# Optimization experiments

Hardware: AMD Instinct MI355X
Metric: run time of the kernel (lower is better)

The kernel has to match this reference:

```python
import jax, jax.numpy as jnp
import numpy as np

S = 64        # state_dim
M = 16        # message_dim
H = 128       # hidden_unit_message_dim
HR = 128      # hidden_unit_readout_dim
NSTEPS = 10
N_NODES = 10000
N_FACTORS = 40000


def setup_inputs() -> dict:
    rng = np.random.default_rng(0)
    n, F = N_NODES, N_FACTORS
    # random undirected factor pairs (u, v) with u < v
    u = rng.integers(0, n - 1, F)
    v = rng.integers(u + 1, n)
    # var->factor directed edges: (u, i) and (v, i) for factor i
    v2f_src = np.stack([u, v], 1).ravel().astype(np.int32)          # [E]
    v2f_dst = np.repeat(np.arange(F), 2).astype(np.int32)           # [E]
    b = rng.normal(size=n).astype(np.float32)
    Juv = rng.normal(size=F).astype(np.float32)
    Jvu = rng.normal(size=F).astype(np.float32)
    feat_u = np.stack([b[u], b[v], Juv, Jvu], 1)
    feat_v = np.stack([b[v], b[u], Juv, Jvu], 1)
    feat = np.stack([feat_u, feat_v], 1).reshape(-1, 4).astype(np.float32)  # [E,4]
    p = lambda *s: (0.1 * rng.normal(size=s)).astype(np.float32)
    z = lambda *s: np.zeros(s, np.float32)
    inp = {
        'v2f_src': jnp.asarray(v2f_src), 'v2f_dst': jnp.asarray(v2f_dst),
        'f2v_src': jnp.asarray(v2f_dst), 'f2v_dst': jnp.asarray(v2f_src),
        'feat_v2f': jnp.asarray(feat), 'feat_f2v': jnp.asarray(feat),
        'n_nodes': n, 'n_factors': F,
        'Qw': jnp.asarray(p(4, M * M)), 'Qb': jnp.asarray(z(M * M)),
        'mp1_w1': jnp.asarray(p(2 * S, H)), 'mp1_b1': jnp.asarray(z(H)),
        'mp1_w2': jnp.asarray(p(H, H)), 'mp1_b2': jnp.asarray(z(H)),
        'mp1_w3': jnp.asarray(p(H, M)), 'mp1_b3': jnp.asarray(z(M)),
        'mp2_w1': jnp.asarray(p(2 * S, H)), 'mp2_b1': jnp.asarray(z(H)),
        'mp2_w2': jnp.asarray(p(H, H)), 'mp2_b2': jnp.asarray(z(H)),
        'mp2_w3': jnp.asarray(p(H, M)), 'mp2_b3': jnp.asarray(z(M)),
        'g1_wih': jnp.asarray(p(M, 3 * S)), 'g1_whh': jnp.asarray(p(S, 3 * S)),
        'g1_bih': jnp.asarray(z(3 * S)), 'g1_bhh': jnp.asarray(z(3 * S)),
        'g2_wih': jnp.asarray(p(M, 3 * S)), 'g2_whh': jnp.asarray(p(S, 3 * S)),
        'g2_bih': jnp.asarray(z(3 * S)), 'g2_bhh': jnp.asarray(z(3 * S)),
        'ro_w1': jnp.asarray(p(S, HR)), 'ro_b1': jnp.asarray(z(HR)),
        'ro_w2': jnp.asarray(p(HR, HR)), 'ro_b2': jnp.asarray(z(HR)),
        'ro_w3': jnp.asarray(p(HR, 2)), 'ro_b3': jnp.asarray(z(2)),
    }
    return inp


def _mlp(x, w1, b1, w2, b2, w3, b3):
    h = jax.nn.relu(x @ w1 + b1)
    h = jax.nn.relu(h @ w2 + b2)
    return h @ w3 + b3


def _gru(x, h, wih, whh, bih, bhh):
    # torch.nn.GRUCell gate order: r, z, n
    gi = x @ wih + bih
    gh = h @ whh + bhh
    ir, iz, inn = jnp.split(gi, 3, axis=-1)
    hr, hz, hn = jnp.split(gh, 3, axis=-1)
    r = jax.nn.sigmoid(ir + hr)
    zg = jax.nn.sigmoid(iz + hz)
    ng = jnp.tanh(inn + r * hn)
    return (1.0 - zg) * ng + zg * h


def reference(v2f_src, v2f_dst, f2v_src, f2v_dst, feat_v2f, feat_f2v,
              n_nodes, n_factors, Qw, Qb,
              mp1_w1, mp1_b1, mp1_w2, mp1_b2, mp1_w3, mp1_b3,
              mp2_w1, mp2_b1, mp2_w2, mp2_b2, mp2_w3, mp2_b3,
              g1_wih, g1_whh, g1_bih, g1_bhh,
              g2_wih, g2_whh, g2_bih, g2_bhh,
              ro_w1, ro_b1, ro_w2, ro_b2, ro_w3, ro_b3):
    var_h = jnp.zeros((n_nodes, S), feat_v2f.dtype)
    fac_h = jnp.zeros((n_factors, S), feat_v2f.dtype)
    # per-edge transform matrices are the same every step; hoist out of the loop
    q1 = (feat_v2f @ Qw + Qb).reshape(-1, M, M)  # [E, M, M]
    q2 = (feat_f2v @ Qw + Qb).reshape(-1, M, M)
    for _ in range(NSTEPS):
        # var -> factor
        x = jnp.concatenate([var_h[v2f_src], fac_h[v2f_dst]], axis=-1)  # [E, 2S]
        m = _mlp(x, mp1_w1, mp1_b1, mp1_w2, mp1_b2, mp1_w3, mp1_b3)    # [E, M]
        m = jnp.einsum('eij,ej->ei', q1, m)
        fac_msg = jax.ops.segment_sum(m, v2f_dst, num_segments=n_factors)
        fac_h = _gru(fac_msg, fac_h, g1_wih, g1_whh, g1_bih, g1_bhh)
        # factor -> var
        x = jnp.concatenate([fac_h[f2v_src], var_h[f2v_dst]], axis=-1)
        m = _mlp(x, mp2_w1, mp2_b1, mp2_w2, mp2_b2, mp2_w3, mp2_b3)
        m = jnp.einsum('eij,ej->ei', q2, m)
        var_msg = jax.ops.segment_sum(m, f2v_dst, num_segments=n_nodes)
        var_h = _gru(var_msg, var_h, g2_wih, g2_whh, g2_bih, g2_bhh)
    out = _mlp(var_h, ro_w1, ro_b1, ro_w2, ro_b2, ro_w3, ro_b3)  # [n_nodes, 2]
    return jax.nn.softmax(out, axis=1)
```

## Files before the change

### kernel.cpp

```cpp
#include <hip/hip_runtime.h>

#define NSTEPS 10

typedef __attribute__((ext_vector_type(8))) short bf16x8;
typedef __attribute__((ext_vector_type(4))) short bf16x4;
typedef __attribute__((ext_vector_type(4))) float f32x4;

__device__ __forceinline__ float sigmoidf_(float x) { return 1.0f / (1.0f + __expf(-x)); }
__device__ __forceinline__ float tanh_fast(float x) {
  const float e = __expf(2.f * x);
  return 1.f - 2.f / (e + 1.f);
}

__device__ __forceinline__ short bf16_(float x) {
  union { float f; unsigned u; } c; c.f = x;
  unsigned r = (c.u + 0x7FFFu + ((c.u >> 16) & 1u)) >> 16;
  return (short)r;
}
__device__ __forceinline__ unsigned pk2_(float a, float b) {
  union { float f; unsigned u; } ca, cb; ca.f = a; cb.f = b;
  return __builtin_amdgcn_perm(cb.u + 0x8000u, ca.u + 0x8000u, 0x07060302u);
}
__device__ __forceinline__ short pk1_(float a) {
  union { float f; unsigned u; } c; c.f = a;
  return (short)((c.u + 0x8000u) >> 16);
}
__device__ __forceinline__ float lo_(unsigned u) { union { unsigned u; float f; } c; c.u = u << 16; return c.f; }
__device__ __forceinline__ float hi_(unsigned u) { union { unsigned u; float f; } c; c.u = u & 0xffff0000u; return c.f; }

__device__ __forceinline__ f32x4 mfma_16x16x32(bf16x8 a, bf16x8 b, f32x4 c) {
  return __builtin_amdgcn_mfma_f32_16x16x32_bf16(a, b, c, 0, 0, 0);
}

struct PackJob { const float* src; int N; int KS; int nchunks; };
struct PackArgs {
  PackJob jb[10];
  const float* Qw; const float* Qb;
  const float* g1wih; const float* g1whh;
  const float* g2wih; const float* g2whh;
};

__global__ __launch_bounds__(256) void k_pack(PackArgs a, short* __restrict__ out, int total) {
  const int g = blockIdx.x * 256 + threadIdx.x;
  if (g >= total) return;
  int c = g >> 9;
  const int r = g & 511;
  const int j = r & 7, n = (r >> 3) & 15, q = (r >> 7) & 3;
  const int kq = q * 8 + j;
  float val = 0.f;
  bool done = false;
  #pragma unroll
  for (int ji = 0; ji < 10; ++ji) {
    if (!done && c < a.jb[ji].nchunks) {
      const int ks = c % a.jb[ji].KS;
      const int nt = c / a.jb[ji].KS;
      const int k = ks * 32 + kq;
      val = a.jb[ji].src[(size_t)k * a.jb[ji].N + nt * 16 + n];
      done = true;
    }
    if (!done) c -= a.jb[ji].nchunks;
  }
  if (!done) {
    if (c < 5) {
      val = 0.f;
      if (kq < 16) val = (c < 4) ? a.Qw[c * 256 + n * 16 + kq] : a.Qb[n * 16 + kq];
    } else {
      c -= 5;
      const float* wih = (c < 48) ? a.g1wih : a.g2wih;
      const float* whh = (c < 48) ? a.g1whh : a.g2whh;
      if (c >= 48) c -= 48;
      const int nt = c / 3, ks = c % 3;
      const int k = ks * 32 + kq;
      const int ng = nt * 16 + n;
      const int gate = ng >> 6, s = ng & 63;
      val = 0.f;
      if (gate == 0) {
        if (k < 16) val = wih[k * 192 + s];
        else if (k < 80) val = whh[(k - 16) * 192 + s];
      } else if (gate == 1) {
        if (k < 16) val = wih[k * 192 + 64 + s];
        else if (k < 80) val = whh[(k - 16) * 192 + 64 + s];
      } else if (gate == 2) {
        if (k < 16) val = wih[k * 192 + 128 + s];
      } else {
        if (k >= 16 && k < 80) val = whh[(k - 16) * 192 + 128 + s];
      }
    }
  }
  out[g] = bf16_(val);
}

__global__ __launch_bounds__(256) void k_dense2(
    const float* __restrict__ X0, const short* __restrict__ W0, short* __restrict__ C0,
    int rows0, int g0,
    const float* __restrict__ X1, const short* __restrict__ W1, short* __restrict__ C1,
    int rows1, float* __restrict__ zeroPtr)
{
  constexpr int KS = 2, K = 64, STR = K + 8;
  __shared__ short Xs[64 * STR];
  const int t = threadIdx.x, lane = t & 63, wave = t >> 6;

  const float* X; const short* Wf; short* C; int rows, rbase;
  if ((int)blockIdx.x < g0) {
    X = X0; Wf = W0; C = C0; rows = rows0; rbase = blockIdx.x * 64;
  } else {
    X = X1; Wf = W1; C = C1; rows = rows1; rbase = ((int)blockIdx.x - g0) * 64;
    if (zeroPtr) {
      const int zr = rbase + (t >> 2);
      if (zr < rows1) {
        f32x4 z = {0.f, 0.f, 0.f, 0.f};
        *(f32x4*)(zeroPtr + (size_t)zr * 16 + (t & 3) * 4) = z;
      }
    }
  }

  bf16x8 b[2][KS];
  #pragma unroll
  for (int nt2 = 0; nt2 < 2; ++nt2)
    #pragma unroll
    for (int ks = 0; ks < KS; ++ks)
      b[nt2][ks] = ((const bf16x8*)Wf)[((wave * 2 + nt2) * KS + ks) * 64 + lane];

  {
    const int r = t >> 2, q4 = t & 3, rg = rbase + r;
    #pragma unroll
    for (int i = 0; i < K / 16; ++i) {
      const int cc = q4 * 4 + i * 16;
      f32x4 v = {0.f, 0.f, 0.f, 0.f};
      if (rg < rows) v = *(const f32x4*)(X + (size_t)rg * K + cc);
      *(unsigned*)&Xs[r * STR + cc]     = pk2_(v.x, v.y);
      *(unsigned*)&Xs[r * STR + cc + 2] = pk2_(v.z, v.w);
    }
  }
  __syncthreads();

  const int m = lane & 15, quad = lane >> 4;
  f32x4 acc[2][4] = {};
  #pragma unroll
  for (int ks = 0; ks < KS; ++ks) {
    bf16x8 afr[4];
    #pragma unroll
    for (int mt = 0; mt < 4; ++mt)
      afr[mt] = *(const bf16x8*)&Xs[(mt * 16 + m) * STR + ks * 32 + quad * 8];
    #pragma unroll
    for (int nt2 = 0; nt2 < 2; ++nt2)
      #pragma unroll
      for (int mt = 0; mt < 4; ++mt)
        acc[nt2][mt] = mfma_16x16x32(afr[mt], b[nt2][ks], acc[nt2][mt]);
  }

  #pragma unroll
  for (int nt2 = 0; nt2 < 2; ++nt2) {
    const int col = (wave * 2 + nt2) * 16 + m;
    #pragma unroll
    for (int mt = 0; mt < 4; ++mt)
      #pragma unroll
      for (int rr = 0; rr < 4; ++rr) {
        const int rg = rbase + mt * 16 + quad * 4 + rr;
        if (rg < rows) C[(size_t)rg * 128 + col] = pk1_(acc[nt2][mt][rr]);
      }
  }
}

template<int KS>
__global__ __launch_bounds__(256) void k_dense(
    const float* __restrict__ X, const short* __restrict__ Wf,
    const float* __restrict__ bias, float* __restrict__ C, int rows)
{
  constexpr int K = KS * 32;
  constexpr int STR = K + 8;
  __shared__ short Xs[64 * STR];
  const int t = threadIdx.x, lane = t & 63, wave = t >> 6;
  const int rbase = blockIdx.x * 64;

  bf16x8 b[2][KS];
  #pragma unroll
  for (int nt2 = 0; nt2 < 2; ++nt2)
    #pragma unroll
    for (int ks = 0; ks < KS; ++ks)
      b[nt2][ks] = ((const bf16x8*)Wf)[((wave * 2 + nt2) * KS + ks) * 64 + lane];

  {
    const int r = t >> 2, q4 = t & 3, rg = rbase + r;
    #pragma unroll
    for (int i = 0; i < K / 16; ++i) {
      const int cc = q4 * 4 + i * 16;
      f32x4 v = {0.f, 0.f, 0.f, 0.f};
      if (rg < rows) v = *(const f32x4*)(X + (size_t)rg * K + cc);
      *(unsigned*)&Xs[r * STR + cc]     = pk2_(v.x, v.y);
      *(unsigned*)&Xs[r * STR + cc + 2] = pk2_(v.z, v.w);
    }
  }
  __syncthreads();

  const int m = lane & 15, quad = lane >> 4;
  f32x4 acc[2][4] = {};
  #pragma unroll
  for (int ks = 0; ks < KS; ++ks) {
    bf16x8 afr[4];
    #pragma unroll
    for (int mt = 0; mt < 4; ++mt)
      afr[mt] = *(const bf16x8*)&Xs[(mt * 16 + m) * STR + ks * 32 + quad * 8];
    #pragma unroll
    for (int nt2 = 0; nt2 < 2; ++nt2)
      #pragma unroll
      for (int mt = 0; mt < 4; ++mt)
        acc[nt2][mt] = mfma_16x16x32(afr[mt], b[nt2][ks], acc[nt2][mt]);
  }

  #pragma unroll
  for (int nt2 = 0; nt2 < 2; ++nt2) {
    const int col = (wave * 2 + nt2) * 16 + m;
    const float bv = bias[col];
    #pragma unroll
    for (int mt = 0; mt < 4; ++mt)
      #pragma unroll
      for (int rr = 0; rr < 4; ++rr) {
        const int rg = rbase + mt * 16 + quad * 4 + rr;
        if (rg < rows) C[(size_t)rg * 128 + col] = fmaxf(acc[nt2][mt][rr] + bv, 0.f);
      }
  }
}

template<bool PAIRED>
__global__ __launch_bounds__(256) void k_edge(
    const short* __restrict__ Pa, const short* __restrict__ Pb,
    const int* __restrict__ src, const int* __restrict__ dst,
    const float* __restrict__ feat,
    const float* __restrict__ b1, const float* __restrict__ b2,
    const float* __restrict__ b3,
    const short* __restrict__ w2f, const short* __restrict__ w3f,
    const short* __restrict__ qf,
    float* __restrict__ outMsg, int E)
{
  __shared__ short h1s[64 * 136];
  __shared__ short ms[64 * 40];
  __shared__ float feats[64 * 4];
  __shared__ int sidx[64], didx[64];

  const int t = threadIdx.x, lane = t & 63, wave = t >> 6;
  const int e0 = blockIdx.x * 64;

  if (t < 64) {
    const int eg = e0 + t;
    sidx[t] = (eg < E) ? src[eg] : 0;
    didx[t] = (eg < E) ? dst[eg] : 0;
  }
  {
    const int e = t >> 2, k = t & 3;
    const int eg = e0 + e;
    feats[e * 4 + k] = (eg < E) ? feat[(size_t)eg * 4 + k] : 0.f;
  }
  bf16x8 bw2[2][4];
  #pragma unroll
  for (int nt2 = 0; nt2 < 2; ++nt2)
    #pragma unroll
    for (int ks = 0; ks < 4; ++ks)
      bw2[nt2][ks] = ((const bf16x8*)w2f)[((wave * 2 + nt2) * 4 + ks) * 64 + lane];
  __syncthreads();

  {
    const int r = t >> 2, q4 = t & 3;
    const bool ok = (e0 + r) < E;
    const short* pa = Pa + (size_t)sidx[r] * 128;
    const short* pb = Pb + (size_t)didx[r] * 128;
    #pragma unroll
    for (int i = 0; i < 4; ++i) {
      const int col = (q4 + i * 4) * 8;
      uint4 o = make_uint4(0u, 0u, 0u, 0u);
      if (ok) {
        const uint4 ua = *(const uint4*)(pa + col);
        const uint4 ub = *(const uint4*)(pb + col);
        const f32x4 ba = *(const f32x4*)(b1 + col);
        const f32x4 bb = *(const f32x4*)(b1 + col + 4);
        o.x = pk2_(fmaxf(lo_(ua.x) + lo_(ub.x) + ba.x, 0.f),
                   fmaxf(hi_(ua.x) + hi_(ub.x) + ba.y, 0.f));
        o.y = pk2_(fmaxf(lo_(ua.y) + lo_(ub.y) + ba.z, 0.f),
                   fmaxf(hi_(ua.y) + hi_(ub.y) + ba.w, 0.f));
        o.z = pk2_(fmaxf(lo_(ua.z) + lo_(ub.z) + bb.x, 0.f),
                   fmaxf(hi_(ua.z) + hi_(ub.z) + bb.y, 0.f));
        o.w = pk2_(fmaxf(lo_(ua.w) + lo_(ub.w) + bb.z, 0.f),
                   fmaxf(hi_(ua.w) + hi_(ub.w) + bb.w, 0.f));
      }
      *(uint4*)&h1s[r * 136 + col] = o;
    }
  }
  __syncthreads();

  const int m = lane & 15, quad = lane >> 4;

  f32x4 acc2[2][4] = {};
  #pragma unroll
  for (int ks = 0; ks < 4; ++ks) {
    bf16x8 afr[4];
    #pragma unroll
    for (int mt = 0; mt < 4; ++mt)
      afr[mt] = *(const bf16x8*)&h1s[(mt * 16 + m) * 136 + ks * 32 + quad * 8];
    #pragma unroll
    for (int nt2 = 0; nt2 < 2; ++nt2)
      #pragma unroll
      for (int mt = 0; mt < 4; ++mt)
        acc2[nt2][mt] = mfma_16x16x32(afr[mt], bw2[nt2][ks], acc2[nt2][mt]);
  }
  __syncthreads();

  #pragma unroll
  for (int nt2 = 0; nt2 < 2; ++nt2) {
    const int col = (wave * 2 + nt2) * 16 + m;
    const float bv = b2[col];
    #pragma unroll
    for (int mt = 0; mt < 4; ++mt)
      #pragma unroll
      for (int rr = 0; rr < 4; ++rr)
        h1s[(mt * 16 + quad * 4 + rr) * 136 + col] =
            pk1_(fmaxf(acc2[nt2][mt][rr] + bv, 0.f));
  }
  bf16x8 bw3[4];
  #pragma unroll
  for (int ks = 0; ks < 4; ++ks) bw3[ks] = ((const bf16x8*)w3f)[ks * 64 + lane];
  bf16x8 bq[5];
  #pragma unroll
  for (int tq = 0; tq < 5; ++tq) bq[tq] = ((const bf16x8*)qf)[tq * 64 + lane];
  __syncthreads();

  f32x4 acc3 = {};
  #pragma unroll
  for (int ks = 0; ks < 4; ++ks) {
    const bf16x8 afr = *(const bf16x8*)&h1s[(wave * 16 + m) * 136 + ks * 32 + quad * 8];
    acc3 = mfma_16x16x32(afr, bw3[ks], acc3);
  }
  const float b3v = b3[m];
  #pragma unroll
  for (int rr = 0; rr < 4; ++rr) {
    const int row = wave * 16 + quad * 4 + rr;
    ms[row * 40 + m] = pk1_(acc3[rr] + b3v);
    ms[row * 40 + 16 + m] = 0;
  }
  __syncthreads();

  f32x4 accY[5] = {};
  {
    const bf16x8 afr = *(const bf16x8*)&ms[(wave * 16 + m) * 40 + quad * 8];
    #pragma unroll
    for (int tq = 0; tq < 5; ++tq) accY[tq] = mfma_16x16x32(afr, bq[tq], accY[tq]);
  }
  float mq[4];
  #pragma unroll
  for (int rr = 0; rr < 4; ++rr) {
    const int row = wave * 16 + quad * 4 + rr;
    const f32x4 f = *(const f32x4*)&feats[row * 4];
    mq[rr] = accY[4][rr] + f.x * accY[0][rr] + f.y * accY[1][rr]
                         + f.z * accY[2][rr] + f.w * accY[3][rr];
  }

  if (PAIRED) {
    const int erow = wave * 16 + quad * 4;
    const int eg = e0 + erow;
    if (eg < E) {
      const int fb = eg >> 1;
      outMsg[(size_t)fb * 16 + m]       = mq[0] + mq[1];
      outMsg[(size_t)(fb + 1) * 16 + m] = mq[2] + mq[3];
    }
  } else {
    #pragma unroll
    for (int rr = 0; rr < 4; ++rr) {
      const int erow = wave * 16 + quad * 4 + rr;
      if (e0 + erow < E)
        atomicAdd(outMsg + (size_t)didx[erow] * 16 + m, mq[rr]);
    }
  }
}

__global__ __launch_bounds__(256) void k_gru(
    const float* __restrict__ msg, float* __restrict__ h,
    const short* __restrict__ Wf,
    const float* __restrict__ bih, const float* __restrict__ bhh, int rows)
{
  __shared__ short As[64 * 104];
  const int t = threadIdx.x, lane = t & 63, wave = t >> 6;
  const int rbase = blockIdx.x * 64;

  {
    const int r = t >> 2, q4 = t & 3, rg = rbase + r;
    #pragma unroll
    for (int i = 0; i < 6; ++i) {
      const int c = (q4 + i * 4) * 4;
      f32x4 v = {0.f, 0.f, 0.f, 0.f};
      if (rg < rows) {
        if (c < 16)      v = *(const f32x4*)(msg + (size_t)rg * 16 + c);
        else if (c < 80) v = *(const f32x4*)(h + (size_t)rg * 64 + (c - 16));
      }
      *(unsigned*)&As[r * 104 + c]     = pk2_(v.x, v.y);
      *(unsigned*)&As[r * 104 + c + 2] = pk2_(v.z, v.w);
    }
  }
  __syncthreads();

  const int m = lane & 15, quad = lane >> 4;
  f32x4 acc[16] = {};
  #pragma unroll
  for (int ks = 0; ks < 3; ++ks) {
    const bf16x8 a = *(const bf16x8*)&As[(wave * 16 + m) * 104 + ks * 32 + quad * 8];
    #pragma unroll
    for (int nt = 0; nt < 16; ++nt) {
      const bf16x8 b = ((const bf16x8*)Wf)[(nt * 3 + ks) * 64 + lane];
      acc[nt] = mfma_16x16x32(a, b, acc[nt]);
    }
  }

  #pragma unroll
  for (int nt = 0; nt < 4; ++nt) {
    const int s = nt * 16 + m;
    const float br  = bih[s] + bhh[s];
    const float bz  = bih[64 + s] + bhh[64 + s];
    const float bin = bih[128 + s];
    const float bhn = bhh[128 + s];
    #pragma unroll
    for (int reg = 0; reg < 4; ++reg) {
      const int rg = rbase + wave * 16 + quad * 4 + reg;
      if (rg < rows) {
        const float ho = h[(size_t)rg * 64 + s];
        const float rr = sigmoidf_(acc[nt][reg] + br);
        const float zz = sigmoidf_(acc[4 + nt][reg] + bz);
        const float nn = tanh_fast(acc[8 + nt][reg] + bin + rr * (acc[12 + nt][reg] + bhn));
        h[(size_t)rg * 64 + s] = (1.f - zz) * nn + zz * ho;
      }
    }
  }
}

__global__ __launch_bounds__(256) void k_readout(
    const float* __restrict__ T2, const float* __restrict__ w3,
    const float* __restrict__ b3, float* __restrict__ out, int rows)
{
  const int n = blockIdx.x * 256 + threadIdx.x;
  if (n >= rows) return;
  float l0 = b3[0], l1 = b3[1];
  #pragma unroll 8
  for (int k = 0; k < 128; k += 4) {
    const float4 x = *(const float4*)(T2 + (size_t)n * 128 + k);
    l0 = fmaf(x.x, w3[(k + 0) * 2 + 0], l0);
    l0 = fmaf(x.y, w3[(k + 1) * 2 + 0], l0);
    l0 = fmaf(x.z, w3[(k + 2) * 2 + 0], l0);
    l0 = fmaf(x.w, w3[(k + 3) * 2 + 0], l0);
    l1 = fmaf(x.x, w3[(k + 0) * 2 + 1], l1);
    l1 = fmaf(x.y, w3[(k + 1) * 2 + 1], l1);
    l1 = fmaf(x.z, w3[(k + 2) * 2 + 1], l1);
    l1 = fmaf(x.w, w3[(k + 3) * 2 + 1], l1);
  }
  const float mx = fmaxf(l0, l1);
  const float e0 = __expf(l0 - mx), e1 = __expf(l1 - mx);
  const float inv = 1.f / (e0 + e1);
  out[(size_t)n * 2 + 0] = e0 * inv;
  out[(size_t)n * 2 + 1] = e1 * inv;
}

extern "C" void kernel_launch(void* const* d_in, const int* in_sizes, int n_in,
                              void* d_out, int out_size, void* d_ws, size_t ws_size,
                              hipStream_t stream)
{
  const int*   v2f_src  = (const int*)d_in[0];
  const int*   v2f_dst  = (const int*)d_in[1];
  const int*   f2v_src  = (const int*)d_in[2];
  const int*   f2v_dst  = (const int*)d_in[3];
  const float* feat_v2f = (const float*)d_in[4];
  const float* feat_f2v = (const float*)d_in[5];
  const float* Qw    = (const float*)d_in[8];
  const float* Qb    = (const float*)d_in[9];
  const float* m1w1  = (const float*)d_in[10];
  const float* m1b1  = (const float*)d_in[11];
  const float* m1w2  = (const float*)d_in[12];
  const float* m1b2  = (const float*)d_in[13];
  const float* m1w3  = (const float*)d_in[14];
  const float* m1b3  = (const float*)d_in[15];
  const float* m2w1  = (const float*)d_in[16];
  const float* m2b1  = (const float*)d_in[17];
  const float* m2w2  = (const float*)d_in[18];
  const float* m2b2  = (const float*)d_in[19];
  const float* m2w3  = (const float*)d_in[20];
  const float* m2b3  = (const float*)d_in[21];
  const float* g1wih = (const float*)d_in[22];
  const float* g1whh = (const float*)d_in[23];
  const float* g1bih = (const float*)d_in[24];
  const float* g1bhh = (const float*)d_in[25];
  const float* g2wih = (const float*)d_in[26];
  const float* g2whh = (const float*)d_in[27];
  const float* g2bih = (const float*)d_in[28];
  const float* g2bhh = (const float*)d_in[29];
  const float* row1  = (const float*)d_in[30];
  const float* rob1  = (const float*)d_in[31];
  const float* row2  = (const float*)d_in[32];
  const float* rob2  = (const float*)d_in[33];
  const float* row3  = (const float*)d_in[34];
  const float* rob3  = (const float*)d_in[35];

  const int E = in_sizes[0];
  const int N = out_size / 2;
  const int F = E / 2;

  float* ws    = (float*)d_ws;
  float* var_h = ws;
  float* fac_h = var_h + (size_t)N * 64;
  float* msgF  = fac_h + (size_t)F * 64;
  float* msgV  = msgF  + (size_t)F * 16;
  float* T1    = msgV  + (size_t)N * 16;
  float* T2    = T1    + (size_t)N * 128;
  short* Abuf  = (short*)(T2 + (size_t)N * 128);
  short* Bbuf  = Abuf + (size_t)F * 128;
  short* wb    = Bbuf + (size_t)F * 128;

  const int C_W2A = 0,  C_W2B = 32, C_W3A = 64, C_W3B = 68;
  const int C_W1AS = 72, C_W1AD = 88, C_W1BS = 104, C_W1BD = 120;
  const int C_RO1 = 136, C_RO2 = 152, C_Q = 184, C_G1 = 189, C_G2 = 237;
  const int TOTAL_CHUNKS = 285;

  short* PB_w2a  = wb + C_W2A  * 512;
  short* PB_w2b  = wb + C_W2B  * 512;
  short* PB_w3a  = wb + C_W3A  * 512;
  short* PB_w3b  = wb + C_W3B  * 512;
  short* PB_w1as = wb + C_W1AS * 512;
  short* PB_w1ad = wb + C_W1AD * 512;
  short* PB_w1bs = wb + C_W1BS * 512;
  short* PB_w1bd = wb + C_W1BD * 512;
  short* PB_ro1  = wb + C_RO1  * 512;
  short* PB_ro2  = wb + C_RO2  * 512;
  short* PB_q    = wb + C_Q    * 512;
  short* PB_g1   = wb + C_G1   * 512;
  short* PB_g2   = wb + C_G2   * 512;

  hipMemsetAsync(var_h, 0, (size_t)N * 64 * sizeof(float), stream);
  hipMemsetAsync(fac_h, 0, (size_t)F * 64 * sizeof(float), stream);

  PackArgs pa;
  pa.jb[0] = {m1w2,            128, 4, 32};
  pa.jb[1] = {m2w2,            128, 4, 32};
  pa.jb[2] = {m1w3,             16, 4,  4};
  pa.jb[3] = {m2w3,             16, 4,  4};
  pa.jb[4] = {m1w1,            128, 2, 16};
  pa.jb[5] = {m1w1 + 64 * 128, 128, 2, 16};
  pa.jb[6] = {m2w1,            128, 2, 16};
  pa.jb[7] = {m2w1 + 64 * 128, 128, 2, 16};
  pa.jb[8] = {row1,            128, 2, 16};
  pa.jb[9] = {row2,            128, 4, 32};
  pa.Qw = Qw; pa.Qb = Qb;
  pa.g1wih = g1wih; pa.g1whh = g1whh;
  pa.g2wih = g2wih; pa.g2whh = g2whh;
  const int packTotal = TOTAL_CHUNKS * 512;
  k_pack<<<(packTotal + 255) / 256, 256, 0, stream>>>(pa, wb, packTotal);

  const int gN = (N + 63) / 64;
  const int gF = (F + 63) / 64;
  const int gE = (E + 63) / 64;

  for (int step = 0; step < NSTEPS; ++step) {
    k_dense2<<<gN + gF, 256, 0, stream>>>(var_h, PB_w1as, Abuf, N, gN,
                                          fac_h, PB_w1ad, Bbuf, F, nullptr);
    k_edge<true><<<gE, 256, 0, stream>>>(Abuf, Bbuf, v2f_src, v2f_dst, feat_v2f,
                                         m1b1, m1b2, m1b3, PB_w2a, PB_w3a, PB_q, msgF, E);
    k_gru<<<gF, 256, 0, stream>>>(msgF, fac_h, PB_g1, g1bih, g1bhh, F);
    k_dense2<<<gF + gN, 256, 0, stream>>>(fac_h, PB_w1bs, Abuf, F, gF,
                                          var_h, PB_w1bd, Bbuf, N, msgV);
    k_edge<false><<<gE, 256, 0, stream>>>(Abuf, Bbuf, f2v_src, f2v_dst, feat_f2v,
                                          m2b1, m2b2, m2b3, PB_w2b, PB_w3b, PB_q, msgV, E);
    k_gru<<<gN, 256, 0, stream>>>(msgV, var_h, PB_g2, g2bih, g2bhh, N);
  }

  k_dense<2><<<gN, 256, 0, stream>>>(var_h, PB_ro1, rob1, T1, N);
  k_dense<4><<<gN, 256, 0, stream>>>(T1,    PB_ro2, rob2, T2, N);
  k_readout<<<(N + 255) / 256, 256, 0, stream>>>(T2, row3, rob3, (float*)d_out, N);
}
```

Before: 825.1 us.

## Fuse GRU updates into edge and dense kernels and fuse readout MLP

The factor GRU now runs at the end of the paired edge kernel. Each block owns 32 consecutive factors, so it can reduce the message pair in LDS and update fac_h directly, with no msgF buffer. The variable GRU is deferred into the job0 blocks of the next step's dense kernel, and the final step's GRU is folded into one readout kernel that also chains the two dense layers and the softmax through LDS. This removes the standalone GRU and readout launches and the global round-trips for msgF, T1 and T2. The cost is more LDS and register pressure per block and extra MFMA work inside the edge kernel.

```diff
diff --git a/kernel.cpp b/kernel.cpp
--- a/kernel.cpp
+++ b/kernel.cpp
@@ -94,14 +94,20 @@
     const float* __restrict__ X0, const short* __restrict__ W0, short* __restrict__ C0,
     int rows0, int g0,
     const float* __restrict__ X1, const short* __restrict__ W1, short* __restrict__ C1,
-    int rows1, float* __restrict__ zeroPtr)
+    int rows1, float* __restrict__ zeroPtr,
+    const float* __restrict__ gruMsg, float* __restrict__ gruH,
+    const short* __restrict__ gruW,
+    const float* __restrict__ gbih, const float* __restrict__ gbhh)
 {
   constexpr int KS = 2, K = 64, STR = K + 8;
   __shared__ short Xs[64 * STR];
+  __shared__ short SA[64 * 104];
   const int t = threadIdx.x, lane = t & 63, wave = t >> 6;
+  const int m = lane & 15, quad = lane >> 4;
 
   const float* X; const short* Wf; short* C; int rows, rbase;
-  if ((int)blockIdx.x < g0) {
+  const bool job0 = (int)blockIdx.x < g0;
+  if (job0) {
     X = X0; Wf = W0; C = C0; rows = rows0; rbase = blockIdx.x * 64;
   } else {
     X = X1; Wf = W1; C = C1; rows = rows1; rbase = ((int)blockIdx.x - g0) * 64;
@@ -121,7 +127,56 @@
     for (int ks = 0; ks < KS; ++ks)
       b[nt2][ks] = ((const bf16x8*)Wf)[((wave * 2 + nt2) * KS + ks) * 64 + lane];
 
-  {
+  if (job0 && gruMsg) {
+    {
+      const int r = t >> 2, q4 = t & 3, rg = rbase + r;
+      #pragma unroll
+      for (int i = 0; i < 6; ++i) {
+        const int c = q4 * 4 + i * 16;
+        f32x4 v = {0.f, 0.f, 0.f, 0.f};
+        if (rg < rows) {
+          if (c < 16)      v = *(const f32x4*)(gruMsg + (size_t)rg * 16 + c);
+          else if (c < 80) v = *(const f32x4*)(gruH + (size_t)rg * 64 + (c - 16));
+        }
+        *(unsigned*)&SA[r * 104 + c]     = pk2_(v.x, v.y);
+        *(unsigned*)&SA[r * 104 + c + 2] = pk2_(v.z, v.w);
+      }
+    }
+    __syncthreads();
+    f32x4 acc[16] = {};
+    #pragma unroll
+    for (int ks = 0; ks < 3; ++ks) {
+      const bf16x8 a = *(const bf16x8*)&SA[(wave * 16 + m) * 104 + ks * 32 + quad * 8];
+      #pragma unroll
+      for (int nt = 0; nt < 16; ++nt)
+        acc[nt] = mfma_16x16x32(a, ((const bf16x8*)gruW)[(nt * 3 + ks) * 64 + lane], acc[nt]);
+    }
+    #pragma unroll
+    for (int nt = 0; nt < 4; ++nt) {
+      const int s = nt * 16 + m;
+      const float br  = gbih[s] + gbhh[s];
+      const float bz  = gbih[64 + s] + gbhh[64 + s];
+      const float bin = gbih[128 + s];
+      const float bhn = gbhh[128 + s];
+      #pragma unroll
+      for (int reg = 0; reg < 4; ++reg) {
+        const int lr = wave * 16 + quad * 4 + reg;
+        const int rg = rbase + lr;
+        short hv = 0;
+        if (rg < rows) {
+          const float ho = gruH[(size_t)rg * 64 + s];
+          const float rr = sigmoidf_(acc[nt][reg] + br);
+          const float zz = sigmoidf_(acc[4 + nt][reg] + bz);
+          const float nn = tanh_fast(acc[8 + nt][reg] + bin + rr * (acc[12 + nt][reg] + bhn));
+          const float hn = (1.f - zz) * nn + zz * ho;
+          gruH[(size_t)rg * 64 + s] = hn;
+          hv = pk1_(hn);
+        }
+        Xs[lr * STR + s] = hv;
+      }
+    }
+    __syncthreads();
+  } else {
     const int r = t >> 2, q4 = t & 3, rg = rbase + r;
     #pragma unroll
     for (int i = 0; i < K / 16; ++i) {
@@ -131,10 +186,9 @@
       *(unsigned*)&Xs[r * STR + cc]     = pk2_(v.x, v.y);
       *(unsigned*)&Xs[r * STR + cc + 2] = pk2_(v.z, v.w);
     }
-  }
-  __syncthreads();
-
-  const int m = lane & 15, quad = lane >> 4;
+    __syncthreads();
+  }
+
   f32x4 acc[2][4] = {};
   #pragma unroll
   for (int ks = 0; ks < KS; ++ks) {
@@ -158,66 +212,6 @@
       for (int rr = 0; rr < 4; ++rr) {
         const int rg = rbase + mt * 16 + quad * 4 + rr;
         if (rg < rows) C[(size_t)rg * 128 + col] = pk1_(acc[nt2][mt][rr]);
-      }
-  }
-}
-
-template<int KS>
-__global__ __launch_bounds__(256) void k_dense(
-    const float* __restrict__ X, const short* __restrict__ Wf,
-    const float* __restrict__ bias, float* __restrict__ C, int rows)
-{
-  constexpr int K = KS * 32;
-  constexpr int STR = K + 8;
-  __shared__ short Xs[64 * STR];
-  const int t = threadIdx.x, lane = t & 63, wave = t >> 6;
-  const int rbase = blockIdx.x * 64;
-
-  bf16x8 b[2][KS];
-  #pragma unroll
-  for (int nt2 = 0; nt2 < 2; ++nt2)
-    #pragma unroll
-    for (int ks = 0; ks < KS; ++ks)
-      b[nt2][ks] = ((const bf16x8*)Wf)[((wave * 2 + nt2) * KS + ks) * 64 + lane];
-
-  {
-    const int r = t >> 2, q4 = t & 3, rg = rbase + r;
-    #pragma unroll
-    for (int i = 0; i < K / 16; ++i) {
-      const int cc = q4 * 4 + i * 16;
-      f32x4 v = {0.f, 0.f, 0.f, 0.f};
-      if (rg < rows) v = *(const f32x4*)(X + (size_t)rg * K + cc);
-      *(unsigned*)&Xs[r * STR + cc]     = pk2_(v.x, v.y);
-      *(unsigned*)&Xs[r * STR + cc + 2] = pk2_(v.z, v.w);
-    }
-  }
-  __syncthreads();
-
-  const int m = lane & 15, quad = lane >> 4;
-  f32x4 acc[2][4] = {};
-  #pragma unroll
-  for (int ks = 0; ks < KS; ++ks) {
-    bf16x8 afr[4];
-    #pragma unroll
-    for (int mt = 0; mt < 4; ++mt)
-      afr[mt] = *(const bf16x8*)&Xs[(mt * 16 + m) * STR + ks * 32 + quad * 8];
-    #pragma unroll
-    for (int nt2 = 0; nt2 < 2; ++nt2)
-      #pragma unroll
-      for (int mt = 0; mt < 4; ++mt)
-        acc[nt2][mt] = mfma_16x16x32(afr[mt], b[nt2][ks], acc[nt2][mt]);
-  }
-
-  #pragma unroll
-  for (int nt2 = 0; nt2 < 2; ++nt2) {
-    const int col = (wave * 2 + nt2) * 16 + m;
-    const float bv = bias[col];
-    #pragma unroll
-    for (int mt = 0; mt < 4; ++mt)
-      #pragma unroll
-      for (int rr = 0; rr < 4; ++rr) {
-        const int rg = rbase + mt * 16 + quad * 4 + rr;
-        if (rg < rows) C[(size_t)rg * 128 + col] = fmaxf(acc[nt2][mt][rr] + bv, 0.f);
       }
   }
 }
@@ -231,15 +225,20 @@
     const float* __restrict__ b3,
     const short* __restrict__ w2f, const short* __restrict__ w3f,
     const short* __restrict__ qf,
-    float* __restrict__ outMsg, int E)
+    float* __restrict__ outMsg,
+    float* __restrict__ facH, const short* __restrict__ gruW,
+    const float* __restrict__ gbih, const float* __restrict__ gbhh,
+    int E, int F)
 {
   __shared__ short h1s[64 * 136];
   __shared__ short ms[64 * 40];
+  __shared__ short AsG[32 * 104];
   __shared__ float feats[64 * 4];
   __shared__ int sidx[64], didx[64];
 
   const int t = threadIdx.x, lane = t & 63, wave = t >> 6;
   const int e0 = blockIdx.x * 64;
+  const int f0 = e0 >> 1;
 
   if (t < 64) {
     const int eg = e0 + t;
@@ -250,6 +249,23 @@
     const int e = t >> 2, k = t & 3;
     const int eg = e0 + e;
     feats[e * 4 + k] = (eg < E) ? feat[(size_t)eg * 4 + k] : 0.f;
+  }
+  if (PAIRED) {
+    const int hr = t >> 3, hc = (t & 7) * 8;
+    const int f = f0 + hr;
+    f32x4 a0 = {0.f,0.f,0.f,0.f}, a1 = {0.f,0.f,0.f,0.f};
+    if (f < F) {
+      a0 = *(const f32x4*)(facH + (size_t)f * 64 + hc);
+      a1 = *(const f32x4*)(facH + (size_t)f * 64 + hc + 4);
+    }
+    uint4 o;
+    o.x = pk2_(a0.x, a0.y); o.y = pk2_(a0.z, a0.w);
+    o.z = pk2_(a1.x, a1.y); o.w = pk2_(a1.z, a1.w);
+    *(uint4*)&AsG[hr * 104 + 16 + hc] = o;
+    if (t < 64) {
+      uint4 z = make_uint4(0u, 0u, 0u, 0u);
+      *(uint4*)&AsG[(t >> 1) * 104 + 80 + (t & 1) * 8] = z;
+    }
   }
   bf16x8 bw2[2][4];
   #pragma unroll
@@ -354,12 +370,46 @@
   }
 
   if (PAIRED) {
-    const int erow = wave * 16 + quad * 4;
-    const int eg = e0 + erow;
-    if (eg < E) {
-      const int fb = eg >> 1;
-      outMsg[(size_t)fb * 16 + m]       = mq[0] + mq[1];
-      outMsg[(size_t)(fb + 1) * 16 + m] = mq[2] + mq[3];
+    {
+      const int fl = wave * 8 + quad * 2;
+      AsG[fl * 104 + m]       = pk1_(mq[0] + mq[1]);
+      AsG[(fl + 1) * 104 + m] = pk1_(mq[2] + mq[3]);
+    }
+    __syncthreads();
+    const int mt = wave >> 1, sh = wave & 1;
+    f32x4 accG[8] = {};
+    #pragma unroll
+    for (int ks = 0; ks < 3; ++ks) {
+      const bf16x8 a = *(const bf16x8*)&AsG[(mt * 16 + m) * 104 + ks * 32 + quad * 8];
+      #pragma unroll
+      for (int g = 0; g < 4; ++g)
+        #pragma unroll
+        for (int nt2 = 0; nt2 < 2; ++nt2) {
+          const int nt = g * 4 + sh * 2 + nt2;
+          accG[g * 2 + nt2] =
+              mfma_16x16x32(a, ((const bf16x8*)gruW)[(nt * 3 + ks) * 64 + lane],
+                            accG[g * 2 + nt2]);
+        }
+    }
+    #pragma unroll
+    for (int nt2 = 0; nt2 < 2; ++nt2) {
+      const int s = sh * 32 + nt2 * 16 + m;
+      const float br  = gbih[s] + gbhh[s];
+      const float bz  = gbih[64 + s] + gbhh[64 + s];
+      const float bin = gbih[128 + s];
+      const float bhn = gbhh[128 + s];
+      #pragma unroll
+      for (int reg = 0; reg < 4; ++reg) {
+        const int f = f0 + mt * 16 + quad * 4 + reg;
+        if (f < F) {
+          const float ho = facH[(size_t)f * 64 + s];
+          const float rr = sigmoidf_(accG[nt2][reg] + br);
+          const float zz = sigmoidf_(accG[2 + nt2][reg] + bz);
+          const float nn = tanh_fast(accG[4 + nt2][reg] + bin +
+                                     rr * (accG[6 + nt2][reg] + bhn));
+          facH[(size_t)f * 64 + s] = (1.f - zz) * nn + zz * ho;
+        }
+      }
     }
   } else {
     #pragma unroll
@@ -371,88 +421,155 @@
   }
 }
 
-__global__ __launch_bounds__(256) void k_gru(
-    const float* __restrict__ msg, float* __restrict__ h,
-    const short* __restrict__ Wf,
-    const float* __restrict__ bih, const float* __restrict__ bhh, int rows)
+__global__ __launch_bounds__(256) void k_readout_f(
+    const float* __restrict__ gruMsg, const float* __restrict__ gruH,
+    const short* __restrict__ gruW,
+    const float* __restrict__ gbih, const float* __restrict__ gbhh,
+    const short* __restrict__ ro1f, const float* __restrict__ rob1,
+    const short* __restrict__ ro2f, const float* __restrict__ rob2,
+    const float* __restrict__ row3, const float* __restrict__ rob3,
+    float* __restrict__ out, int rows)
 {
-  __shared__ short As[64 * 104];
+  __shared__ short SA[64 * 104];
+  __shared__ short SH[64 * 72];
+  __shared__ short S1[64 * 136];
+  __shared__ short S2[64 * 136];
+  __shared__ float w3s[256];
   const int t = threadIdx.x, lane = t & 63, wave = t >> 6;
+  const int m = lane & 15, quad = lane >> 4;
   const int rbase = blockIdx.x * 64;
+
+  w3s[t] = row3[t];
 
   {
     const int r = t >> 2, q4 = t & 3, rg = rbase + r;
     #pragma unroll
     for (int i = 0; i < 6; ++i) {
-      const int c = (q4 + i * 4) * 4;
+      const int c = q4 * 4 + i * 16;
       f32x4 v = {0.f, 0.f, 0.f, 0.f};
       if (rg < rows) {
-        if (c < 16)      v = *(const f32x4*)(msg + (size_t)rg * 16 + c);
-        else if (c < 80) v = *(const f32x4*)(h + (size_t)rg * 64 + (c - 16));
-      }
-      *(unsigned*)&As[r * 104 + c]     = pk2_(v.x, v.y);
-      *(unsigned*)&As[r * 104 + c + 2] = pk2_(v.z, v.w);
-    }
-  }
-  __syncthreads();
-
-  const int m = lane & 15, quad = lane >> 4;
-  f32x4 acc[16] = {};
-  #pragma unroll
-  for (int ks = 0; ks < 3; ++ks) {
-    const bf16x8 a = *(const bf16x8*)&As[(wave * 16 + m) * 104 + ks * 32 + quad * 8];
-    #pragma unroll
-    for (int nt = 0; nt < 16; ++nt) {
-      const bf16x8 b = ((const bf16x8*)Wf)[(nt * 3 + ks) * 64 + lane];
-      acc[nt] = mfma_16x16x32(a, b, acc[nt]);
-    }
-  }
-
-  #pragma unroll
-  for (int nt = 0; nt < 4; ++nt) {
-    const int s = nt * 16 + m;
-    const float br  = bih[s] + bhh[s];
-    const float bz  = bih[64 + s] + bhh[64 + s];
-    const float bin = bih[128 + s];
-    const float bhn = bhh[128 + s];
-    #pragma unroll
-    for (int reg = 0; reg < 4; ++reg) {
-      const int rg = rbase + wave * 16 + quad * 4 + reg;
-      if (rg < rows) {
-        const float ho = h[(size_t)rg * 64 + s];
-        const float rr = sigmoidf_(acc[nt][reg] + br);
-        const float zz = sigmoidf_(acc[4 + nt][reg] + bz);
-        const float nn = tanh_fast(acc[8 + nt][reg] + bin + rr * (acc[12 + nt][reg] + bhn));
-        h[(size_t)rg * 64 + s] = (1.f - zz) * nn + zz * ho;
-      }
-    }
-  }
-}
-
-__global__ __launch_bounds__(256) void k_readout(
-    const float* __restrict__ T2, const float* __restrict__ w3,
-    const float* __restrict__ b3, float* __restrict__ out, int rows)
-{
-  const int n = blockIdx.x * 256 + threadIdx.x;
-  if (n >= rows) return;
-  float l0 = b3[0], l1 = b3[1];
-  #pragma unroll 8
-  for (int k = 0; k < 128; k += 4) {
-    const float4 x = *(const float4*)(T2 + (size_t)n * 128 + k);
-    l0 = fmaf(x.x, w3[(k + 0) * 2 + 0], l0);
-    l0 = fmaf(x.y, w3[(k + 1) * 2 + 0], l0);
-    l0 = fmaf(x.z, w3[(k + 2) * 2 + 0], l0);
-    l0 = fmaf(x.w, w3[(k + 3) * 2 + 0], l0);
-    l1 = fmaf(x.x, w3[(k + 0) * 2 + 1], l1);
-    l1 = fmaf(x.y, w3[(k + 1) * 2 + 1], l1);
-    l1 = fmaf(x.z, w3[(k + 2) * 2 + 1], l1);
-    l1 = fmaf(x.w, w3[(k + 3) * 2 + 1], l1);
-  }
-  const float mx = fmaxf(l0, l1);
-  const float e0 = __expf(l0 - mx), e1 = __expf(l1 - mx);
-  const float inv = 1.f / (e0 + e1);
-  out[(size_t)n * 2 + 0] = e0 * inv;
-  out[(size_t)n * 2 + 1] = e1 * inv;
+        if (c < 16)      v = *(const f32x4*)(gruMsg + (size_t)rg * 16 + c);
+        else if (c < 80) v = *(const f32x4*)(gruH + (size_t)rg * 64 + (c - 16));
+      }
+      *(unsigned*)&SA[r * 104 + c]     = pk2_(v.x, v.y);
+      *(unsigned*)&SA[r * 104 + c + 2] = pk2_(v.z, v.w);
+    }
+  }
+  __syncthreads();
+  {
+    f32x4 acc[16] = {};
+    #pragma unroll
+    for (int ks = 0; ks < 3; ++ks) {
+      const bf16x8 a = *(const bf16x8*)&SA[(wave * 16 + m) * 104 + ks * 32 + quad * 8];
+      #pragma unroll
+      for (int nt = 0; nt < 16; ++nt)
+        acc[nt] = mfma_16x16x32(a, ((const bf16x8*)gruW)[(nt * 3 + ks) * 64 + lane], acc[nt]);
+    }
+    #pragma unroll
+    for (int nt = 0; nt < 4; ++nt) {
+      const int s = nt * 16 + m;
+      const float br  = gbih[s] + gbhh[s];
+      const float bz  = gbih[64 + s] + gbhh[64 + s];
+      const float bin = gbih[128 + s];
+      const float bhn = gbhh[128 + s];
+      #pragma unroll
+      for (int reg = 0; reg < 4; ++reg) {
+        const int lr = wave * 16 + quad * 4 + reg;
+        const int rg = rbase + lr;
+        short hv = 0;
+        if (rg < rows) {
+          const float ho = gruH[(size_t)rg * 64 + s];
+          const float rr = sigmoidf_(acc[nt][reg] + br);
+          const float zz = sigmoidf_(acc[4 + nt][reg] + bz);
+          const float nn = tanh_fast(acc[8 + nt][reg] + bin + rr * (acc[12 + nt][reg] + bhn));
+          hv = pk1_((1.f - zz) * nn + zz * ho);
+        }
+        SH[lr * 72 + s] = hv;
+      }
+    }
+  }
+  __syncthreads();
+
+  {
+    f32x4 acc[2][4] = {};
+    #pragma unroll
+    for (int ks = 0; ks < 2; ++ks) {
+      bf16x8 afr[4];
+      #pragma unroll
+      for (int mt = 0; mt < 4; ++mt)
+        afr[mt] = *(const bf16x8*)&SH[(mt * 16 + m) * 72 + ks * 32 + quad * 8];
+      #pragma unroll
+      for (int nt2 = 0; nt2 < 2; ++nt2) {
+        const bf16x8 bb = ((const bf16x8*)ro1f)[((wave * 2 + nt2) * 2 + ks) * 64 + lane];
+        #pragma unroll
+        for (int mt = 0; mt < 4; ++mt)
+          acc[nt2][mt] = mfma_16x16x32(afr[mt], bb, acc[nt2][mt]);
+      }
+    }
+    #pragma unroll
+    for (int nt2 = 0; nt2 < 2; ++nt2) {
+      const int col = (wave * 2 + nt2) * 16 + m;
+      const float bv = rob1[col];
+      #pragma unroll
+      for (int mt = 0; mt < 4; ++mt)
+        #pragma unroll
+        for (int rr = 0; rr < 4; ++rr)
+          S1[(mt * 16 + quad * 4 + rr) * 136 + col] =
+              pk1_(fmaxf(acc[nt2][mt][rr] + bv, 0.f));
+    }
+  }
+  __syncthreads();
+
+  {
+    f32x4 acc[2][4] = {};
+    #pragma unroll
+    for (int ks = 0; ks < 4; ++ks) {
+      bf16x8 afr[4];
+      #pragma unroll
+      for (int mt = 0; mt < 4; ++mt)
+        afr[mt] = *(const bf16x8*)&S1[(mt * 16 + m) * 136 + ks * 32 + quad * 8];
+      #pragma unroll
+      for (int nt2 = 0; nt2 < 2; ++nt2) {
+        const bf16x8 bb = ((const bf16x8*)ro2f)[((wave * 2 + nt2) * 4 + ks) * 64 + lane];
+        #pragma unroll
+        for (int mt = 0; mt < 4; ++mt)
+          acc[nt2][mt] = mfma_16x16x32(afr[mt], bb, acc[nt2][mt]);
+      }
+    }
+    #pragma unroll
+    for (int nt2 = 0; nt2 < 2; ++nt2) {
+      const int col = (wave * 2 + nt2) * 16 + m;
+      const float bv = rob2[col];
+      #pragma unroll
+      for (int mt = 0; mt < 4; ++mt)
+        #pragma unroll
+        for (int rr = 0; rr < 4; ++rr)
+          S2[(mt * 16 + quad * 4 + rr) * 136 + col] =
+              pk1_(fmaxf(acc[nt2][mt][rr] + bv, 0.f));
+    }
+  }
+  __syncthreads();
+
+  if (t < 64) {
+    const int rg = rbase + t;
+    if (rg < rows) {
+      float l0 = rob3[0], l1 = rob3[1];
+      #pragma unroll 8
+      for (int k = 0; k < 128; k += 2) {
+        const unsigned u = *(const unsigned*)&S2[t * 136 + k];
+        const float x0 = lo_(u), x1 = hi_(u);
+        l0 = fmaf(x0, w3s[k * 2 + 0], l0);
+        l1 = fmaf(x0, w3s[k * 2 + 1], l1);
+        l0 = fmaf(x1, w3s[k * 2 + 2], l0);
+        l1 = fmaf(x1, w3s[k * 2 + 3], l1);
+      }
+      const float mx = fmaxf(l0, l1);
+      const float e0 = __expf(l0 - mx), e1 = __expf(l1 - mx);
+      const float inv = 1.f / (e0 + e1);
+      out[(size_t)rg * 2 + 0] = e0 * inv;
+      out[(size_t)rg * 2 + 1] = e1 * inv;
+    }
+  }
 }
 
 extern "C" void kernel_launch(void* const* d_in, const int* in_sizes, int n_in,
@@ -501,11 +618,8 @@
   float* ws    = (float*)d_ws;
   float* var_h = ws;
   float* fac_h = var_h + (size_t)N * 64;
-  float* msgF  = fac_h + (size_t)F * 64;
-  float* msgV  = msgF  + (size_t)F * 16;
-  float* T1    = msgV  + (size_t)N * 16;
-  float* T2    = T1    + (size_t)N * 128;
-  short* Abuf  = (short*)(T2 + (size_t)N * 128);
+  float* msgV  = fac_h + (size_t)F * 64;
+  short* Abuf  = (short*)(msgV + (size_t)N * 16);
   short* Bbuf  = Abuf + (size_t)F * 128;
   short* wb    = Bbuf + (size_t)F * 128;
 
@@ -553,19 +667,23 @@
   const int gE = (E + 63) / 64;
 
   for (int step = 0; step < NSTEPS; ++step) {
-    k_dense2<<<gN + gF, 256, 0, stream>>>(var_h, PB_w1as, Abuf, N, gN,
-                                          fac_h, PB_w1ad, Bbuf, F, nullptr);
-    k_edge<true><<<gE, 256, 0, stream>>>(Abuf, Bbuf, v2f_src, v2f_dst, feat_v2f,
-                                         m1b1, m1b2, m1b3, PB_w2a, PB_w3a, PB_q, msgF, E);
-    k_gru<<<gF, 256, 0, stream>>>(msgF, fac_h, PB_g1, g1bih, g1bhh, F);
-    k_dense2<<<gF + gN, 256, 0, stream>>>(fac_h, PB_w1bs, Abuf, F, gF,
-                                          var_h, PB_w1bd, Bbuf, N, msgV);
-    k_edge<false><<<gE, 256, 0, stream>>>(Abuf, Bbuf, f2v_src, f2v_dst, feat_f2v,
-                                          m2b1, m2b2, m2b3, PB_w2b, PB_w3b, PB_q, msgV, E);
-    k_gru<<<gN, 256, 0, stream>>>(msgV, var_h, PB_g2, g2bih, g2bhh, N);
-  }
-
-  k_dense<2><<<gN, 256, 0, stream>>>(var_h, PB_ro1, rob1, T1, N);
-  k_dense<4><<<gN, 256, 0, stream>>>(T1,    PB_ro2, rob2, T2, N);
-  k_readout<<<(N + 255) / 256, 256, 0, stream>>>(T2, row3, rob3, (float*)d_out, N);
-}
+    k_dense2<<<gN + gF, 256, 0, stream>>>(
+        var_h, PB_w1as, Abuf, N, gN,
+        fac_h, PB_w1ad, Bbuf, F, nullptr,
+        step ? msgV : nullptr, var_h, PB_g2, g2bih, g2bhh);
+    k_edge<true><<<gE, 256, 0, stream>>>(
+        Abuf, Bbuf, v2f_src, v2f_dst, feat_v2f, m1b1, m1b2, m1b3,
+        PB_w2a, PB_w3a, PB_q, nullptr, fac_h, PB_g1, g1bih, g1bhh, E, F);
+    k_dense2<<<gF + gN, 256, 0, stream>>>(
+        fac_h, PB_w1bs, Abuf, F, gF,
+        var_h, PB_w1bd, Bbuf, N, msgV,
+        nullptr, nullptr, nullptr, nullptr, nullptr);
+    k_edge<false><<<gE, 256, 0, stream>>>(
+        Abuf, Bbuf, f2v_src, f2v_dst, feat_f2v, m2b1, m2b2, m2b3,
+        PB_w2b, PB_w3b, PB_q, msgV, nullptr, nullptr, nullptr, nullptr, E, F);
+  }
+
+  k_readout_f<<<gN, 256, 0, stream>>>(
+      msgV, var_h, PB_g2, g2bih, g2bhh,
+      PB_ro1, rob1, PB_ro2, rob2, row3, rob3, (float*)d_out, N);
+}
```

Result: faster. 717.1 us (-13.1%).
